# Performance work log

Hardware: AMD Instinct MI355X
Metric: run time of the kernel (lower is better)

Reference implementation:

```python
import jax, jax.numpy as jnp
import numpy as np

B = 64          # graphs per batch
N = 131072      # total nodes (B * 2048)
E = 524288      # total edges
V = 32000       # embedding vocab
D_IN = 256      # embed.output_size
D = 128         # GCN hidden size


def setup_inputs() -> dict:
    key = jax.random.key(0)
    ks = jax.random.split(key, 9)
    return {
        "node_tokens": jax.random.randint(ks[0], (N,), 0, V),
        "edge_index": jax.random.randint(ks[1], (2, E), 0, N),
        "embed_table": jax.random.normal(ks[2], (V, D_IN), jnp.float32),
        "W_node_w": jax.random.normal(ks[3], (D, D_IN), jnp.float32) * 0.02,
        "W_node_b": jax.random.normal(ks[4], (D,), jnp.float32) * 0.02,
        "conv1_w": jax.random.normal(ks[5], (D, D), jnp.float32) * 0.02,
        "conv1_b": jax.random.normal(ks[6], (D,), jnp.float32) * 0.02,
        "conv2_w": jax.random.normal(ks[7], (D, D), jnp.float32) * 0.02,
        "conv2_b": jax.random.normal(ks[8], (D,), jnp.float32) * 0.02,
    }


def _gcn_conv(x, src, dst, norm, W, b):
    # PyG GCNConv: linear first, then normalized scatter-add aggregation, then bias.
    x = x @ W.T                                        # [N, D]
    msg = x[src] * norm[:, None]                       # gather + per-edge scale
    out = jax.ops.segment_sum(msg, dst, num_segments=N)  # scatter-add at dst
    return out + b


def reference(node_tokens, edge_index, embed_table, W_node_w, W_node_b,
              conv1_w, conv1_b, conv2_w, conv2_b):
    # compute_node_features: embed lookup -> W_node linear (no mask path)
    x = embed_table[node_tokens] @ W_node_w.T + W_node_b   # [N, D]

    # GCNConv normalization with self-loops (shared by both layers)
    loop = jnp.arange(N)
    src = jnp.concatenate([edge_index[0], loop])
    dst = jnp.concatenate([edge_index[1], loop])
    deg = jax.ops.segment_sum(jnp.ones(E + N, x.dtype), dst, num_segments=N)
    dinv = jnp.where(deg > 0, jax.lax.rsqrt(deg), 0.0)
    norm = dinv[src] * dinv[dst]                           # [E+N]

    x = jax.nn.relu(_gcn_conv(x, src, dst, norm, conv1_w, conv1_b))
    x = _gcn_conv(x, src, dst, norm, conv2_w, conv2_b)

    # Unpad into [B, max_n, D]; equal-length graphs, no edge tokens -> reshape.
    n = N // B
    output = x.reshape(B, n, D)          # dropout_p=0 -> identity
    labels = node_tokens.reshape(B, n)
    labels_mask = jnp.ones((B, n), dtype=bool)
    label_node_ids = jnp.broadcast_to(jnp.arange(n), (B, n))
    return output, labels, labels_mask, label_node_ids
```

## Files before the change

kernel.cpp:

```cpp
#include <hip/hip_runtime.h>
#include <hip/hip_bf16.h>

#define N_NODES 131072
#define N_EDGES 524288
#define DHID    128
#define DIN     256
#define VOCAB   32000

typedef __attribute__((ext_vector_type(8))) short short8;
typedef __attribute__((ext_vector_type(4))) float floatx4;

__device__ inline short bf16_rne(float f) {
    union { float f; unsigned u; } v; v.f = f;
    unsigned r = v.u + 0x7FFF + ((v.u >> 16) & 1);
    return (short)(r >> 16);
}
__device__ inline float bf16_to_f(short s) {
    union { unsigned u; float f; } v; v.u = ((unsigned)(unsigned short)s) << 16;
    return v.f;
}
__device__ inline short8 cvt8(float4 lo, float4 hi) {
    short8 o;
    o[0] = bf16_rne(lo.x); o[1] = bf16_rne(lo.y);
    o[2] = bf16_rne(lo.z); o[3] = bf16_rne(lo.w);
    o[4] = bf16_rne(hi.x); o[5] = bf16_rne(hi.y);
    o[6] = bf16_rne(hi.z); o[7] = bf16_rne(hi.w);
    return o;
}


__global__ __launch_bounds__(256) void count_edges(const int* __restrict__ edst,
                                                   int* __restrict__ counts) {
    int i = blockIdx.x * 256 + threadIdx.x;
    int4 e = ((const int4*)edst)[i];
    atomicAdd(&counts[e.x], 1);
    atomicAdd(&counts[e.y], 1);
    atomicAdd(&counts[e.z], 1);
    atomicAdd(&counts[e.w], 1);
}


__global__ __launch_bounds__(256) void alloc_csr(const int* __restrict__ counts,
                                                 int* __restrict__ offsets,
                                                 int* __restrict__ cursor,
                                                 float* __restrict__ dinv,
                                                 int* __restrict__ total,
                                                 const int* __restrict__ tok,
                                                 float* __restrict__ meta_out) {
    __shared__ int s[256];
    __shared__ int base;
    int i = blockIdx.x * 256 + threadIdx.x;
    int v = counts[i];
    s[threadIdx.x] = v;
    __syncthreads();
    for (int d = 1; d < 256; d <<= 1) {
        int t = (threadIdx.x >= d) ? s[threadIdx.x - d] : 0;
        __syncthreads();
        s[threadIdx.x] += t;
        __syncthreads();
    }
    int incl = s[threadIdx.x];
    if (threadIdx.x == 255) base = atomicAdd(total, incl);
    __syncthreads();
    int off = base + incl - v;
    offsets[i] = off;
    cursor[i]  = off;
    dinv[i] = rsqrtf((float)(v + 1));

    const size_t L0 = (size_t)N_NODES * DHID;
    __builtin_nontemporal_store((float)tok[i],     &meta_out[L0 + i]);
    __builtin_nontemporal_store(1.0f,              &meta_out[L0 + N_NODES + i]);
    __builtin_nontemporal_store((float)(i & 2047), &meta_out[L0 + 2 * N_NODES + i]);
}


#define FG_GEMM  250
#define FG_WCONV 128
#define FG_FILL  (N_EDGES / 256)
#define FG_TOTAL (FG_GEMM + FG_WCONV + FG_FILL)

__global__ __launch_bounds__(256) void fill_gemm(const float* __restrict__ emb,
                                                 const float* __restrict__ Wn,
                                                 short* __restrict__ z,
                                                 const float* __restrict__ W1,
                                                 const float* __restrict__ W2,
                                                 short* __restrict__ W1b,
                                                 short* __restrict__ W2b,
                                                 const int* __restrict__ src,
                                                 const int* __restrict__ dst,
                                                 int* __restrict__ cursor,
                                                 const int* __restrict__ counts,
                                                 const int* __restrict__ tok,
                                                 int2* __restrict__ csr) {
    const int b = blockIdx.x;
    if (b < FG_GEMM) {
        const int t = threadIdx.x;
        const int wid  = t >> 6;
        const int lane = t & 63;
        const int col  = lane & 15;
        const int quad = lane >> 4;
        const int vbase = b * 128 + wid * 32;
        const size_t row0 = (size_t)(vbase + col);
        const size_t row1 = (size_t)(vbase + 16 + col);

        floatx4 acc[2][8] = {};
#pragma unroll
        for (int kc = 0; kc < DIN / 32; ++kc) {
            const int ko = kc * 32 + quad * 8;
            short8 a0 = cvt8(*(const float4*)&emb[row0 * DIN + ko],
                             *(const float4*)&emb[row0 * DIN + ko + 4]);
            short8 a1 = cvt8(*(const float4*)&emb[row1 * DIN + ko],
                             *(const float4*)&emb[row1 * DIN + ko + 4]);
#pragma unroll
            for (int ft = 0; ft < 8; ++ft) {
                const size_t wr = (size_t)(col * 8 + ft) * DIN + ko;
                short8 bb = cvt8(*(const float4*)&Wn[wr],
                                 *(const float4*)&Wn[wr + 4]);
                acc[0][ft] = __builtin_amdgcn_mfma_f32_16x16x32_bf16(a0, bb, acc[0][ft], 0, 0, 0);
                acc[1][ft] = __builtin_amdgcn_mfma_f32_16x16x32_bf16(a1, bb, acc[1][ft], 0, 0, 0);
            }
        }
#pragma unroll
        for (int mt = 0; mt < 2; ++mt) {
#pragma unroll
            for (int r = 0; r < 4; ++r) {
                const int row = vbase + mt * 16 + quad * 4 + r;
                short8 o;
#pragma unroll
                for (int ft = 0; ft < 8; ++ft)
                    o[ft] = bf16_rne(acc[mt][ft][r]);
                *(short8*)&z[(size_t)row * DHID + col * 8] = o;
            }
        }
    } else if (b < FG_GEMM + FG_WCONV) {
        int i = (b - FG_GEMM) * 256 + threadIdx.x;
        if (i < 16384) W1b[i] = bf16_rne(W1[i]);
        else           W2b[i - 16384] = bf16_rne(W2[i - 16384]);
    } else {
        int e = (b - FG_GEMM - FG_WCONV) * 256 + threadIdx.x;
        int d = dst[e];
        int s = src[e];
        int p = atomicAdd(&cursor[d], 1);
        int deg = counts[s];
        csr[p] = make_int2((deg << 24) | tok[s],
                           (deg << 24) | s);
    }
}


template <bool RELU, bool OUT_BF16, bool ZG>
__global__ __launch_bounds__(256, 8) void fused_conv(const short* __restrict__ x,
                                                     const int2* __restrict__ csr,
                                                     const int* __restrict__ offsets,
                                                     const int* __restrict__ counts,
                                                     const float* __restrict__ dinv,
                                                     const int* __restrict__ tok,
                                                     const float* __restrict__ bn,
                                                     const short* __restrict__ Wb,
                                                     const float* __restrict__ bias,
                                                     void* __restrict__ outp) {
    const int t = threadIdx.x;
    const int wid  = t >> 6;
    const int lane = t & 63;
    const int col  = lane & 15;
    const int quad = lane >> 4;
    const int base = (blockIdx.x * 4 + wid) * 16;
    const int node = base + col;

    const float di = dinv[node];
    const int beg = offsets[node];
    const int cnt = counts[node];
    const int2* pcsr = csr + beg;

    float af[4][8];
    {
        const int self = ZG ? tok[node] : node;
        const size_t xrow = (size_t)self * DHID + quad * 8;
#pragma unroll
        for (int c = 0; c < 4; ++c) {
            short8 v = *(const short8*)&x[xrow + c * 32];
#pragma unroll
            for (int j = 0; j < 8; ++j) af[c][j] = di * bf16_to_f(v[j]);
        }
    }
    float sw = di;

    int2 cn = (cnt > 0) ? pcsr[0] : make_int2(0, 0);
    for (int e = 0; e < cnt; ++e) {
        const int   ce = ZG ? cn.x : cn.y;
        const int   s  = ce & 0xFFFFFF;
        const float w  = rsqrtf((float)(((unsigned)ce >> 24) + 1));
        if (e + 1 < cnt) cn = pcsr[e + 1];
        if (ZG) sw += w;
        const size_t r0 = (size_t)s * DHID + quad * 8;
        short8 u0 = *(const short8*)&x[r0];
        short8 u1 = *(const short8*)&x[r0 + 32];
        short8 u2 = *(const short8*)&x[r0 + 64];
        short8 u3 = *(const short8*)&x[r0 + 96];
#pragma unroll
        for (int j = 0; j < 8; ++j) {
            af[0][j] = fmaf(w, bf16_to_f(u0[j]), af[0][j]);
            af[1][j] = fmaf(w, bf16_to_f(u1[j]), af[1][j]);
            af[2][j] = fmaf(w, bf16_to_f(u2[j]), af[2][j]);
            af[3][j] = fmaf(w, bf16_to_f(u3[j]), af[3][j]);
        }
    }

    short8 a[4];
#pragma unroll
    for (int c = 0; c < 4; ++c) {
        if (ZG) {
            const float4 b0 = *(const float4*)&bn[c * 32 + quad * 8];
            const float4 b1 = *(const float4*)&bn[c * 32 + quad * 8 + 4];
            const float bv[8] = {b0.x, b0.y, b0.z, b0.w, b1.x, b1.y, b1.z, b1.w};
#pragma unroll
            for (int j = 0; j < 8; ++j)
                a[c][j] = bf16_rne(di * (af[c][j] + sw * bv[j]));
        } else {
#pragma unroll
            for (int j = 0; j < 8; ++j) a[c][j] = bf16_rne(di * af[c][j]);
        }
    }

    floatx4 acc[8] = {};
#pragma unroll
    for (int c = 0; c < 4; ++c) {
        const int ko = c * 32 + quad * 8;
#pragma unroll
        for (int ft = 0; ft < 8; ++ft) {
            short8 b = *(const short8*)&Wb[(size_t)(col * 8 + ft) * DHID + ko];
            acc[ft] = __builtin_amdgcn_mfma_f32_16x16x32_bf16(a[c], b, acc[ft], 0, 0, 0);
        }
    }

    const float4 bv0 = *(const float4*)&bias[col * 8];
    const float4 bv1 = *(const float4*)&bias[col * 8 + 4];
    const float bb[8] = {bv0.x, bv0.y, bv0.z, bv0.w, bv1.x, bv1.y, bv1.z, bv1.w};
    short* outb = (short*)outp;
    float* outf = (float*)outp;
#pragma unroll
    for (int r = 0; r < 4; ++r) {
        const size_t row = (size_t)(base + quad * 4 + r) * DHID + col * 8;
        if (OUT_BF16) {
            short8 o;
#pragma unroll
            for (int ft = 0; ft < 8; ++ft) {
                float v = acc[ft][r] + bb[ft];
                if (RELU) v = fmaxf(v, 0.f);
                o[ft] = bf16_rne(v);
            }
            *(short8*)&outb[row] = o;
        } else {
            floatx4 o0, o1;
            o0[0] = acc[0][r] + bb[0]; o0[1] = acc[1][r] + bb[1];
            o0[2] = acc[2][r] + bb[2]; o0[3] = acc[3][r] + bb[3];
            o1[0] = acc[4][r] + bb[4]; o1[1] = acc[5][r] + bb[5];
            o1[2] = acc[6][r] + bb[6]; o1[3] = acc[7][r] + bb[7];
            if (RELU) {
#pragma unroll
                for (int k = 0; k < 4; ++k) {
                    o0[k] = fmaxf(o0[k], 0.f);
                    o1[k] = fmaxf(o1[k], 0.f);
                }
            }
            __builtin_nontemporal_store(o0, (floatx4*)&outf[row]);
            __builtin_nontemporal_store(o1, (floatx4*)&outf[row + 4]);
        }
    }
}


extern "C" void kernel_launch(void* const* d_in, const int* in_sizes, int n_in,
                              void* d_out, int out_size, void* d_ws, size_t ws_size,
                              hipStream_t stream) {
    const int*   tok  = (const int*)d_in[0];
    const int*   esrc = (const int*)d_in[1];
    const int*   edst = esrc + N_EDGES;
    const float* emb  = (const float*)d_in[2];
    const float* Wn   = (const float*)d_in[3];
    const float* bn   = (const float*)d_in[4];
    const float* W1   = (const float*)d_in[5];
    const float* b1   = (const float*)d_in[6];
    const float* W2   = (const float*)d_in[7];
    const float* b2   = (const float*)d_in[8];
    float* out = (float*)d_out;

    char* ws = (char*)d_ws;
    int*   counts  = (int*)(ws);
    int*   total   = (int*)(ws + (1u << 19));
    int*   offsets = (int*)(ws + (1u << 19) + 256);
    int*   cursor  = (int*)(ws + (2u << 19) + 256);
    float* dinv    = (float*)(ws + (3u << 19) + 256);
    int2*  csr     = (int2*)(ws + 3 * (1u << 20));
    short* W1b     = (short*)(ws + 7 * (1u << 20));
    short* W2b     = (short*)(ws + 7 * (1u << 20) + (1u << 15));
    short* z       = (short*)(ws + 8 * (1u << 20));
    short* x2b     = (short*)(ws + 16 * (1u << 20));

    hipMemsetAsync(counts, 0, (1u << 19) + 256, stream);
    count_edges<<<N_EDGES / 1024, 256, 0, stream>>>(edst, counts);
    alloc_csr<<<N_NODES / 256, 256, 0, stream>>>(counts, offsets, cursor, dinv,
                                                 total, tok, out);
    fill_gemm<<<FG_TOTAL, 256, 0, stream>>>(emb, Wn, z, W1, W2, W1b, W2b,
                                            esrc, edst, cursor, counts, tok, csr);

    fused_conv<true, true, true><<<N_NODES / 64, 256, 0, stream>>>(
        z, csr, offsets, counts, dinv, tok, bn, W1b, b1, x2b);
    fused_conv<false, false, false><<<N_NODES / 64, 256, 0, stream>>>(
        x2b, csr, offsets, counts, dinv, tok, bn, W2b, b2, out);
}
```

Baseline: 296.2 us.

## Split layer-1 vocab gathers into three passes and pack degree with token

The first conv layer now makes three passes over each node's edge list. Each pass gathers only neighbours whose token id falls in one third of the vocabulary, so that part of the projected vocab table can stay resident in cache. The edge-fill step reads a single precomputed degree|token word per source instead of two separate lookups, and the layer-1 bf16 output uses nontemporal stores. The cost is reading the CSR three times and taking divergent branches per edge, which may outweigh any cache gain.

```diff
diff --git a/kernel.cpp b/kernel.cpp
--- a/kernel.cpp
+++ b/kernel.cpp
@@ -44,6 +44,7 @@
                                                  int* __restrict__ offsets,
                                                  int* __restrict__ cursor,
                                                  float* __restrict__ dinv,
+                                                 int* __restrict__ ptk,
                                                  int* __restrict__ total,
                                                  const int* __restrict__ tok,
                                                  float* __restrict__ meta_out) {
@@ -66,9 +67,11 @@
     offsets[i] = off;
     cursor[i]  = off;
     dinv[i] = rsqrtf((float)(v + 1));
+    int tk = tok[i];
+    ptk[i] = (v << 24) | tk;
 
     const size_t L0 = (size_t)N_NODES * DHID;
-    __builtin_nontemporal_store((float)tok[i],     &meta_out[L0 + i]);
+    __builtin_nontemporal_store((float)tk,         &meta_out[L0 + i]);
     __builtin_nontemporal_store(1.0f,              &meta_out[L0 + N_NODES + i]);
     __builtin_nontemporal_store((float)(i & 2047), &meta_out[L0 + 2 * N_NODES + i]);
 }
@@ -89,8 +92,7 @@
                                                  const int* __restrict__ src,
                                                  const int* __restrict__ dst,
                                                  int* __restrict__ cursor,
-                                                 const int* __restrict__ counts,
-                                                 const int* __restrict__ tok,
+                                                 const int* __restrict__ ptk,
                                                  int2* __restrict__ csr) {
     const int b = blockIdx.x;
     if (b < FG_GEMM) {
@@ -141,9 +143,8 @@
         int d = dst[e];
         int s = src[e];
         int p = atomicAdd(&cursor[d], 1);
-        int deg = counts[s];
-        csr[p] = make_int2((deg << 24) | tok[s],
-                           (deg << 24) | s);
+        int pt = ptk[s];
+        csr[p] = make_int2(pt, (pt & 0xFF000000) | s);
     }
 }
 
@@ -172,37 +173,74 @@
     const int cnt = counts[node];
     const int2* pcsr = csr + beg;
 
-    float af[4][8];
-    {
-        const int self = ZG ? tok[node] : node;
-        const size_t xrow = (size_t)self * DHID + quad * 8;
-#pragma unroll
-        for (int c = 0; c < 4; ++c) {
-            short8 v = *(const short8*)&x[xrow + c * 32];
-#pragma unroll
-            for (int j = 0; j < 8; ++j) af[c][j] = di * bf16_to_f(v[j]);
-        }
-    }
+    float af[4][8] = {};
     float sw = di;
 
-    int2 cn = (cnt > 0) ? pcsr[0] : make_int2(0, 0);
-    for (int e = 0; e < cnt; ++e) {
-        const int   ce = ZG ? cn.x : cn.y;
-        const int   s  = ce & 0xFFFFFF;
-        const float w  = rsqrtf((float)(((unsigned)ce >> 24) + 1));
-        if (e + 1 < cnt) cn = pcsr[e + 1];
-        if (ZG) sw += w;
-        const size_t r0 = (size_t)s * DHID + quad * 8;
-        short8 u0 = *(const short8*)&x[r0];
-        short8 u1 = *(const short8*)&x[r0 + 32];
-        short8 u2 = *(const short8*)&x[r0 + 64];
-        short8 u3 = *(const short8*)&x[r0 + 96];
-#pragma unroll
-        for (int j = 0; j < 8; ++j) {
-            af[0][j] = fmaf(w, bf16_to_f(u0[j]), af[0][j]);
-            af[1][j] = fmaf(w, bf16_to_f(u1[j]), af[1][j]);
-            af[2][j] = fmaf(w, bf16_to_f(u2[j]), af[2][j]);
-            af[3][j] = fmaf(w, bf16_to_f(u3[j]), af[3][j]);
+    if constexpr (ZG) {
+        const int selftok = tok[node];
+        const int PR = (VOCAB + 2) / 3;
+#pragma unroll 1
+        for (int p = 0; p < 3; ++p) {
+            const int lo = p * PR;
+            const int hi = lo + PR;
+            if (selftok >= lo && selftok < hi) {
+                const size_t xrow = (size_t)selftok * DHID + quad * 8;
+#pragma unroll
+                for (int c = 0; c < 4; ++c) {
+                    short8 v = *(const short8*)&x[xrow + c * 32];
+#pragma unroll
+                    for (int j = 0; j < 8; ++j)
+                        af[c][j] = fmaf(di, bf16_to_f(v[j]), af[c][j]);
+                }
+            }
+            for (int e = 0; e < cnt; ++e) {
+                const int ce = ((const int*)pcsr)[2 * e];
+                const int s  = ce & 0xFFFFFF;
+                if (s >= lo && s < hi) {
+                    const float w = rsqrtf((float)(((unsigned)ce >> 24) + 1));
+                    sw += w;
+                    const size_t r0 = (size_t)s * DHID + quad * 8;
+                    short8 u0 = *(const short8*)&x[r0];
+                    short8 u1 = *(const short8*)&x[r0 + 32];
+                    short8 u2 = *(const short8*)&x[r0 + 64];
+                    short8 u3 = *(const short8*)&x[r0 + 96];
+#pragma unroll
+                    for (int j = 0; j < 8; ++j) {
+                        af[0][j] = fmaf(w, bf16_to_f(u0[j]), af[0][j]);
+                        af[1][j] = fmaf(w, bf16_to_f(u1[j]), af[1][j]);
+                        af[2][j] = fmaf(w, bf16_to_f(u2[j]), af[2][j]);
+                        af[3][j] = fmaf(w, bf16_to_f(u3[j]), af[3][j]);
+                    }
+                }
+            }
+        }
+    } else {
+        {
+            const size_t xrow = (size_t)node * DHID + quad * 8;
+#pragma unroll
+            for (int c = 0; c < 4; ++c) {
+                short8 v = *(const short8*)&x[xrow + c * 32];
+#pragma unroll
+                for (int j = 0; j < 8; ++j) af[c][j] = di * bf16_to_f(v[j]);
+            }
+        }
+        int cn = (cnt > 0) ? ((const int*)pcsr)[1] : 0;
+        for (int e = 0; e < cnt; ++e) {
+            const int   s = cn & 0xFFFFFF;
+            const float w = rsqrtf((float)(((unsigned)cn >> 24) + 1));
+            if (e + 1 < cnt) cn = ((const int*)pcsr)[2 * e + 3];
+            const size_t r0 = (size_t)s * DHID + quad * 8;
+            short8 u0 = *(const short8*)&x[r0];
+            short8 u1 = *(const short8*)&x[r0 + 32];
+            short8 u2 = *(const short8*)&x[r0 + 64];
+            short8 u3 = *(const short8*)&x[r0 + 96];
+#pragma unroll
+            for (int j = 0; j < 8; ++j) {
+                af[0][j] = fmaf(w, bf16_to_f(u0[j]), af[0][j]);
+                af[1][j] = fmaf(w, bf16_to_f(u1[j]), af[1][j]);
+                af[2][j] = fmaf(w, bf16_to_f(u2[j]), af[2][j]);
+                af[3][j] = fmaf(w, bf16_to_f(u3[j]), af[3][j]);
+            }
         }
     }
 
@@ -249,7 +287,7 @@
                 if (RELU) v = fmaxf(v, 0.f);
                 o[ft] = bf16_rne(v);
             }
-            *(short8*)&outb[row] = o;
+            __builtin_nontemporal_store(o, (short8*)&outb[row]);
         } else {
             floatx4 o0, o1;
             o0[0] = acc[0][r] + bb[0]; o0[1] = acc[1][r] + bb[1];
@@ -291,6 +329,7 @@
     int*   offsets = (int*)(ws + (1u << 19) + 256);
     int*   cursor  = (int*)(ws + (2u << 19) + 256);
     float* dinv    = (float*)(ws + (3u << 19) + 256);
+    int*   ptk     = (int*)(ws + (4u << 19) + 256);
     int2*  csr     = (int2*)(ws + 3 * (1u << 20));
     short* W1b     = (short*)(ws + 7 * (1u << 20));
     short* W2b     = (short*)(ws + 7 * (1u << 20) + (1u << 15));
@@ -300,9 +339,9 @@
     hipMemsetAsync(counts, 0, (1u << 19) + 256, stream);
     count_edges<<<N_EDGES / 1024, 256, 0, stream>>>(edst, counts);
     alloc_csr<<<N_NODES / 256, 256, 0, stream>>>(counts, offsets, cursor, dinv,
-                                                 total, tok, out);
+                                                 ptk, total, tok, out);
     fill_gemm<<<FG_TOTAL, 256, 0, stream>>>(emb, Wn, z, W1, W2, W1b, W2b,
-                                            esrc, edst, cursor, counts, tok, csr);
+                                            esrc, edst, cursor, ptk, csr);
 
     fused_conv<true, true, true><<<N_NODES / 64, 256, 0, stream>>>(
         z, csr, offsets, counts, dinv, tok, bn, W1b, b1, x2b);
```

After: 301.5 us. Within noise of the previous version (+1.8%).

## Move GEMM into edge-count kernel and precompute packed degree-token array for CSR fill

Applied to the files above, without the earlier changes.

The embedding GEMM and weight conversion now run in the same launch as the edge degree counting, instead of alongside the CSR fill. The CSR fill becomes its own kernel. It reads a per-node packed (degree<<24 | token) word that alloc_csr precomputes, replacing two separate gathers of counts and tok. Edge counting now uses one edge per thread instead of four, which adds blocks to that launch.

```diff
diff --git a/kernel.cpp b/kernel.cpp
--- a/kernel.cpp
+++ b/kernel.cpp
@@ -29,14 +29,68 @@
 }
 
 
-__global__ __launch_bounds__(256) void count_edges(const int* __restrict__ edst,
-                                                   int* __restrict__ counts) {
-    int i = blockIdx.x * 256 + threadIdx.x;
-    int4 e = ((const int4*)edst)[i];
-    atomicAdd(&counts[e.x], 1);
-    atomicAdd(&counts[e.y], 1);
-    atomicAdd(&counts[e.z], 1);
-    atomicAdd(&counts[e.w], 1);
+#define MG_GEMM  250
+#define MG_WCONV 128
+#define MG_COUNT (N_EDGES / 256)
+#define MG_TOTAL (MG_GEMM + MG_WCONV + MG_COUNT)
+
+__global__ __launch_bounds__(256) void mega(const float* __restrict__ emb,
+                                            const float* __restrict__ Wn,
+                                            short* __restrict__ z,
+                                            const float* __restrict__ W1,
+                                            const float* __restrict__ W2,
+                                            short* __restrict__ W1b,
+                                            short* __restrict__ W2b,
+                                            const int* __restrict__ edst,
+                                            int* __restrict__ counts) {
+    const int b = blockIdx.x;
+    if (b < MG_GEMM) {
+        const int t = threadIdx.x;
+        const int wid  = t >> 6;
+        const int lane = t & 63;
+        const int col  = lane & 15;
+        const int quad = lane >> 4;
+        const int vbase = b * 128 + wid * 32;
+        const size_t row0 = (size_t)(vbase + col);
+        const size_t row1 = (size_t)(vbase + 16 + col);
+
+        floatx4 acc[2][8] = {};
+#pragma unroll
+        for (int kc = 0; kc < DIN / 32; ++kc) {
+            const int ko = kc * 32 + quad * 8;
+            short8 a0 = cvt8(*(const float4*)&emb[row0 * DIN + ko],
+                             *(const float4*)&emb[row0 * DIN + ko + 4]);
+            short8 a1 = cvt8(*(const float4*)&emb[row1 * DIN + ko],
+                             *(const float4*)&emb[row1 * DIN + ko + 4]);
+#pragma unroll
+            for (int ft = 0; ft < 8; ++ft) {
+                const size_t wr = (size_t)(col * 8 + ft) * DIN + ko;
+                short8 bb = cvt8(*(const float4*)&Wn[wr],
+                                 *(const float4*)&Wn[wr + 4]);
+                acc[0][ft] = __builtin_amdgcn_mfma_f32_16x16x32_bf16(a0, bb, acc[0][ft], 0, 0, 0);
+                acc[1][ft] = __builtin_amdgcn_mfma_f32_16x16x32_bf16(a1, bb, acc[1][ft], 0, 0, 0);
+            }
+        }
+#pragma unroll
+        for (int mt = 0; mt < 2; ++mt) {
+#pragma unroll
+            for (int r = 0; r < 4; ++r) {
+                const int row = vbase + mt * 16 + quad * 4 + r;
+                short8 o;
+#pragma unroll
+                for (int ft = 0; ft < 8; ++ft)
+                    o[ft] = bf16_rne(acc[mt][ft][r]);
+                *(short8*)&z[(size_t)row * DHID + col * 8] = o;
+            }
+        }
+    } else if (b < MG_GEMM + MG_WCONV) {
+        int i = (b - MG_GEMM) * 256 + threadIdx.x;
+        if (i < 16384) W1b[i] = bf16_rne(W1[i]);
+        else           W2b[i - 16384] = bf16_rne(W2[i - 16384]);
+    } else {
+        int e = (b - MG_GEMM - MG_WCONV) * 256 + threadIdx.x;
+        atomicAdd(&counts[edst[e]], 1);
+    }
 }
 
 
@@ -44,6 +98,7 @@
                                                  int* __restrict__ offsets,
                                                  int* __restrict__ cursor,
                                                  float* __restrict__ dinv,
+                                                 int* __restrict__ ptk,
                                                  int* __restrict__ total,
                                                  const int* __restrict__ tok,
                                                  float* __restrict__ meta_out) {
@@ -66,85 +121,27 @@
     offsets[i] = off;
     cursor[i]  = off;
     dinv[i] = rsqrtf((float)(v + 1));
+    int tk = tok[i];
+    ptk[i] = (v << 24) | tk;
 
     const size_t L0 = (size_t)N_NODES * DHID;
-    __builtin_nontemporal_store((float)tok[i],     &meta_out[L0 + i]);
+    __builtin_nontemporal_store((float)tk,         &meta_out[L0 + i]);
     __builtin_nontemporal_store(1.0f,              &meta_out[L0 + N_NODES + i]);
     __builtin_nontemporal_store((float)(i & 2047), &meta_out[L0 + 2 * N_NODES + i]);
 }
 
 
-#define FG_GEMM  250
-#define FG_WCONV 128
-#define FG_FILL  (N_EDGES / 256)
-#define FG_TOTAL (FG_GEMM + FG_WCONV + FG_FILL)
-
-__global__ __launch_bounds__(256) void fill_gemm(const float* __restrict__ emb,
-                                                 const float* __restrict__ Wn,
-                                                 short* __restrict__ z,
-                                                 const float* __restrict__ W1,
-                                                 const float* __restrict__ W2,
-                                                 short* __restrict__ W1b,
-                                                 short* __restrict__ W2b,
-                                                 const int* __restrict__ src,
-                                                 const int* __restrict__ dst,
-                                                 int* __restrict__ cursor,
-                                                 const int* __restrict__ counts,
-                                                 const int* __restrict__ tok,
-                                                 int2* __restrict__ csr) {
-    const int b = blockIdx.x;
-    if (b < FG_GEMM) {
-        const int t = threadIdx.x;
-        const int wid  = t >> 6;
-        const int lane = t & 63;
-        const int col  = lane & 15;
-        const int quad = lane >> 4;
-        const int vbase = b * 128 + wid * 32;
-        const size_t row0 = (size_t)(vbase + col);
-        const size_t row1 = (size_t)(vbase + 16 + col);
-
-        floatx4 acc[2][8] = {};
-#pragma unroll
-        for (int kc = 0; kc < DIN / 32; ++kc) {
-            const int ko = kc * 32 + quad * 8;
-            short8 a0 = cvt8(*(const float4*)&emb[row0 * DIN + ko],
-                             *(const float4*)&emb[row0 * DIN + ko + 4]);
-            short8 a1 = cvt8(*(const float4*)&emb[row1 * DIN + ko],
-                             *(const float4*)&emb[row1 * DIN + ko + 4]);
-#pragma unroll
-            for (int ft = 0; ft < 8; ++ft) {
-                const size_t wr = (size_t)(col * 8 + ft) * DIN + ko;
-                short8 bb = cvt8(*(const float4*)&Wn[wr],
-                                 *(const float4*)&Wn[wr + 4]);
-                acc[0][ft] = __builtin_amdgcn_mfma_f32_16x16x32_bf16(a0, bb, acc[0][ft], 0, 0, 0);
-                acc[1][ft] = __builtin_amdgcn_mfma_f32_16x16x32_bf16(a1, bb, acc[1][ft], 0, 0, 0);
-            }
-        }
-#pragma unroll
-        for (int mt = 0; mt < 2; ++mt) {
-#pragma unroll
-            for (int r = 0; r < 4; ++r) {
-                const int row = vbase + mt * 16 + quad * 4 + r;
-                short8 o;
-#pragma unroll
-                for (int ft = 0; ft < 8; ++ft)
-                    o[ft] = bf16_rne(acc[mt][ft][r]);
-                *(short8*)&z[(size_t)row * DHID + col * 8] = o;
-            }
-        }
-    } else if (b < FG_GEMM + FG_WCONV) {
-        int i = (b - FG_GEMM) * 256 + threadIdx.x;
-        if (i < 16384) W1b[i] = bf16_rne(W1[i]);
-        else           W2b[i - 16384] = bf16_rne(W2[i - 16384]);
-    } else {
-        int e = (b - FG_GEMM - FG_WCONV) * 256 + threadIdx.x;
-        int d = dst[e];
-        int s = src[e];
-        int p = atomicAdd(&cursor[d], 1);
-        int deg = counts[s];
-        csr[p] = make_int2((deg << 24) | tok[s],
-                           (deg << 24) | s);
-    }
+__global__ __launch_bounds__(256) void fill_csr(const int* __restrict__ src,
+                                                const int* __restrict__ dst,
+                                                int* __restrict__ cursor,
+                                                const int* __restrict__ ptk,
+                                                int2* __restrict__ csr) {
+    int e = blockIdx.x * 256 + threadIdx.x;
+    int d = dst[e];
+    int s = src[e];
+    int p = atomicAdd(&cursor[d], 1);
+    int pt = ptk[s];
+    csr[p] = make_int2(pt, (pt & 0xFF000000) | s);
 }
 
 
@@ -291,6 +288,7 @@
     int*   offsets = (int*)(ws + (1u << 19) + 256);
     int*   cursor  = (int*)(ws + (2u << 19) + 256);
     float* dinv    = (float*)(ws + (3u << 19) + 256);
+    int*   ptk     = (int*)(ws + (4u << 19) + 256);
     int2*  csr     = (int2*)(ws + 3 * (1u << 20));
     short* W1b     = (short*)(ws + 7 * (1u << 20));
     short* W2b     = (short*)(ws + 7 * (1u << 20) + (1u << 15));
@@ -298,11 +296,10 @@
     short* x2b     = (short*)(ws + 16 * (1u << 20));
 
     hipMemsetAsync(counts, 0, (1u << 19) + 256, stream);
-    count_edges<<<N_EDGES / 1024, 256, 0, stream>>>(edst, counts);
+    mega<<<MG_TOTAL, 256, 0, stream>>>(emb, Wn, z, W1, W2, W1b, W2b, edst, counts);
     alloc_csr<<<N_NODES / 256, 256, 0, stream>>>(counts, offsets, cursor, dinv,
-                                                 total, tok, out);
-    fill_gemm<<<FG_TOTAL, 256, 0, stream>>>(emb, Wn, z, W1, W2, W1b, W2b,
-                                            esrc, edst, cursor, counts, tok, csr);
+                                                 ptk, total, tok, out);
+    fill_csr<<<N_EDGES / 256, 256, 0, stream>>>(esrc, edst, cursor, ptk, csr);
 
     fused_conv<true, true, true><<<N_NODES / 64, 256, 0, stream>>>(
         z, csr, offsets, counts, dinv, tok, bn, W1b, b1, x2b);
```

New measurement: 286.2 us. 1.03x faster.
